# Kernel tuning notes

Hardware: AMD Instinct MI355X
Metric: run time of the kernel (lower is better)

The kernel has to match this reference:

```python
import jax, jax.numpy as jnp
import numpy as np

EPS = 1e-5
L = 8      # n_layers
H = 1024   # n_hidden
F_IN = 26  # input features
B = 65536  # batch


def layer_norm(x, gamma, beta):
    m = jnp.mean(x, axis=-1, keepdims=True)
    v = jnp.mean((x - m) ** 2, axis=-1, keepdims=True)
    return (x - m) * jax.lax.rsqrt(v + EPS) * gamma + beta


def setup_inputs() -> dict:
    key = jax.random.key(0)
    ks = jax.random.split(key, 12)
    s_in = 1.0 / np.sqrt(F_IN)
    s_h = 1.0 / np.sqrt(H)
    return {
        "x": jax.random.normal(ks[0], (B, F_IN), jnp.float32),
        "st_gamma": jnp.ones((F_IN,), jnp.float32),
        "st_beta": jnp.zeros((F_IN,), jnp.float32),
        "st_w": jax.random.uniform(ks[1], (H, F_IN), jnp.float32, -s_in, s_in),
        "st_b": jax.random.uniform(ks[2], (H,), jnp.float32, -s_in, s_in),
        "blk_gamma": jnp.ones((L, H), jnp.float32),
        "blk_beta": jnp.zeros((L, H), jnp.float32),
        "blk_w": jax.random.uniform(ks[3], (L, H, H), jnp.float32, -s_h, s_h),
        "blk_b": jax.random.uniform(ks[4], (L, H), jnp.float32, -s_h, s_h),
        "last_gamma": jnp.ones((H,), jnp.float32),
        "last_beta": jnp.zeros((H,), jnp.float32),
        "last_w": jax.random.uniform(ks[5], (1, H), jnp.float32, -s_h, s_h),
        "last_b": jax.random.uniform(ks[6], (1,), jnp.float32, -s_h, s_h),
    }


def reference(x, st_gamma, st_beta, st_w, st_b,
              blk_gamma, blk_beta, blk_w, blk_b,
              last_gamma, last_beta, last_w, last_b):
    # Stem: LN(26) -> Linear(26->H) -> ReLU (dropout = identity in eval)
    h = jax.nn.relu(layer_norm(x, st_gamma, st_beta) @ st_w.T + st_b)

    # n_layers blocks: LN -> Linear(H->H) -> ReLU, scanned over stacked params
    def body(h, params):
        g, b, w, bb = params
        h = jax.nn.relu(layer_norm(h, g, b) @ w.T + bb)
        return h, None

    h, _ = jax.lax.scan(body, h, (blk_gamma, blk_beta, blk_w, blk_b))

    # Head: LN -> Linear(H->1) -> sigmoid
    h = layer_norm(h, last_gamma, last_beta)
    out = jax.nn.sigmoid(h @ last_w.T + last_b)  # [B, 1]
    return out
```

## Files before the change

kernel.cpp:

```cpp
#include <hip/hip_runtime.h>
#include <hip/hip_bf16.h>
#include <stdint.h>


typedef __attribute__((ext_vector_type(8))) _Float16 f16x8;
typedef __attribute__((ext_vector_type(4))) float f32x4;

#define EPSLN 1e-5f
#define HDIM 1024

__device__ __forceinline__ void gload16(const void* g, void* l) {
  __builtin_amdgcn_global_load_lds(
      (const __attribute__((address_space(1))) unsigned int*)g,
      (__attribute__((address_space(3))) unsigned int*)l, 16, 0, 0);
}

__global__ __launch_bounds__(256) void zero_f32(float* __restrict__ p, int n) {
  int i = blockIdx.x * 256 + threadIdx.x;
  if (i < n) p[i] = 0.f;
}

__global__ __launch_bounds__(256) void fold_blk(
    const float* __restrict__ bg, const float* __restrict__ bb,
    const float* __restrict__ bw, const float* __restrict__ bbias,
    _Float16* __restrict__ Wf, float* __restrict__ bfold, float* __restrict__ Sfold) {
  int lo = blockIdx.x;
  int layer = lo >> 10;
  const float* wrow = bw + (size_t)lo * HDIM;
  const float* g = bg + (size_t)layer * HDIM;
  const float* be = bb + (size_t)layer * HDIM;
  _Float16* wout = Wf + (size_t)lo * HDIM;
  int t = threadIdx.x;
  float s = 0.f, acb = 0.f;
  for (int i = t; i < HDIM; i += 256) {
    float wv = wrow[i];
    _Float16 wp = (_Float16)(wv * g[i]);
    wout[i] = wp;
    s += (float)wp;
    acb += be[i] * wv;
  }
#pragma unroll
  for (int off = 1; off < 64; off <<= 1) { s += __shfl_xor(s, off); acb += __shfl_xor(acb, off); }
  __shared__ float rs[4], rb[4];
  int l = t & 63, w = t >> 6;
  if (l == 0) { rs[w] = s; rb[w] = acb; }
  __syncthreads();
  if (t == 0) {
    Sfold[lo] = rs[0] + rs[1] + rs[2] + rs[3];
    bfold[lo] = bbias[lo] + rb[0] + rb[1] + rb[2] + rb[3];
  }
}

__global__ __launch_bounds__(256) void fold_head(
    const float* __restrict__ lg, const float* __restrict__ lb,
    const float* __restrict__ lw, const float* __restrict__ lbias,
    float* __restrict__ headW, float* __restrict__ headAux) {
  int t = threadIdx.x;
  float s = 0.f, acb = 0.f;
  for (int i = t; i < HDIM; i += 256) {
    float wp = lw[i] * lg[i];
    headW[i] = wp;
    s += wp;
    acb += lb[i] * lw[i];
  }
#pragma unroll
  for (int off = 1; off < 64; off <<= 1) { s += __shfl_xor(s, off); acb += __shfl_xor(acb, off); }
  __shared__ float rs[4], rb[4];
  int l = t & 63, w = t >> 6;
  if (l == 0) { rs[w] = s; rb[w] = acb; }
  __syncthreads();
  if (t == 0) {
    headAux[0] = rs[0] + rs[1] + rs[2] + rs[3];
    headAux[1] = lbias[0] + rb[0] + rb[1] + rb[2] + rb[3];
  }
}

__global__ __launch_bounds__(256) void fold_stem(const float* __restrict__ stw,
                                                 _Float16* __restrict__ Wst) {
  int idx = blockIdx.x * 256 + threadIdx.x;
  int o = idx >> 6, i = idx & 63;
  Wst[idx] = (i < 26) ? (_Float16)stw[o * 26 + i] : (_Float16)0.f;
}

__global__ __launch_bounds__(256) void stem_prep(
    const float* __restrict__ x, const float* __restrict__ stg, const float* __restrict__ stb,
    _Float16* __restrict__ xn, int rowBase) {
  __shared__ float xin[256 * 26];
  __shared__ _Float16 xo[256 * 64];
  int t = threadIdx.x;
  const float* src = x + ((size_t)rowBase + (size_t)blockIdx.x * 256) * 26;
  for (int i = t; i < 256 * 26; i += 256) xin[i] = src[i];
  __syncthreads();
  {
    float m = 0.f;
#pragma unroll
    for (int i = 0; i < 26; ++i) m += xin[t * 26 + i];
    m *= (1.f / 26.f);
    float v = 0.f;
#pragma unroll
    for (int i = 0; i < 26; ++i) { float d = xin[t * 26 + i] - m; v += d * d; }
    float rstd = rsqrtf(v * (1.f / 26.f) + EPSLN);
    _Float16* orow = xo + t * 64;
#pragma unroll
    for (int i = 0; i < 26; ++i)
      orow[i] = (_Float16)((xin[t * 26 + i] - m) * rstd * stg[i] + stb[i]);
#pragma unroll
    for (int i = 26; i < 64; ++i) orow[i] = (_Float16)0.f;
  }
  __syncthreads();
  const float4* s4 = (const float4*)xo;
  float4* d4 = (float4*)(xn + (size_t)blockIdx.x * 256 * 64);
  for (int i = t; i < 2048; i += 256) d4[i] = s4[i];
}

__global__ __launch_bounds__(256) void stem_gemm(
    const _Float16* __restrict__ xn, const _Float16* __restrict__ Wst,
    const float* __restrict__ stbias, _Float16* __restrict__ hout,
    float* __restrict__ stats_out) {
  __shared__ _Float16 As[128 * 64];
  __shared__ _Float16 Bs[128 * 64];
  const int t = threadIdx.x;
  const int l = t & 63;
  const int w = t >> 6;
  const int wm = w >> 1, wn = w & 1;
  const int brow = blockIdx.x * 128;
  const int bcol = blockIdx.y * 128;

  f32x4 acc[4][4];
#pragma unroll
  for (int i = 0; i < 4; ++i)
#pragma unroll
    for (int j = 0; j < 4; ++j) acc[i][j] = (f32x4){0.f, 0.f, 0.f, 0.f};

  const _Float16* ga = xn + (size_t)(brow + (t >> 3)) * 64 + (t & 7) * 8;
  const _Float16* gb = Wst + (size_t)(bcol + (t >> 3)) * 64 + (t & 7) * 8;
  char* lA = (char*)As + (size_t)w * 1024;
  char* lB = (char*)Bs + (size_t)w * 1024;
#pragma unroll
  for (int q = 0; q < 4; ++q) {
    gload16(ga + (size_t)q * 32 * 64, lA + q * 4096);
    gload16(gb + (size_t)q * 32 * 64, lB + q * 4096);
  }
  __syncthreads();

  const int abyte0 = (wm * 64 + (l & 15)) * 128 + (l >> 4) * 16;
  const int bbyte0 = (wn * 64 + (l & 15)) * 128 + (l >> 4) * 16;
#pragma unroll
  for (int ks = 0; ks < 2; ++ks) {
    f16x8 af[4], bfr[4];
#pragma unroll
    for (int m = 0; m < 4; ++m)
      af[m] = *(const f16x8*)((const char*)As + abyte0 + m * 2048 + ks * 64);
#pragma unroll
    for (int n = 0; n < 4; ++n)
      bfr[n] = *(const f16x8*)((const char*)Bs + bbyte0 + n * 2048 + ks * 64);
#pragma unroll
    for (int m = 0; m < 4; ++m)
#pragma unroll
      for (int n = 0; n < 4; ++n)
        acc[m][n] = __builtin_amdgcn_mfma_f32_16x16x32_f16(af[m], bfr[n], acc[m][n], 0, 0, 0);
  }

  __syncthreads();
  float* sred = (float*)As;
  sred[t] = 0.f;
  __syncthreads();

  float Bf[4];
#pragma unroll
  for (int n = 0; n < 4; ++n) Bf[n] = stbias[bcol + wn * 64 + n * 16 + (l & 15)];
#pragma unroll
  for (int m = 0; m < 4; ++m) {
#pragma unroll
    for (int rg = 0; rg < 4; ++rg) {
      int rloc = wm * 64 + m * 16 + (l >> 4) * 4 + rg;
      int lrow = brow + rloc;
      float ps = 0.f, psq = 0.f;
#pragma unroll
      for (int n = 0; n < 4; ++n) {
        int col = bcol + wn * 64 + n * 16 + (l & 15);
        float vv = fmaxf(acc[m][n][rg] + Bf[n], 0.f);
        hout[(size_t)lrow * HDIM + col] = (_Float16)vv;
        ps += vv; psq += vv * vv;
      }
#pragma unroll
      for (int off = 1; off < 16; off <<= 1) {
        ps += __shfl_xor(ps, off);
        psq += __shfl_xor(psq, off);
      }
      if ((l & 15) == 0) {
        atomicAdd(&sred[rloc * 2 + 0], ps);
        atomicAdd(&sred[rloc * 2 + 1], psq);
      }
    }
  }
  __syncthreads();
  atomicAdd(&stats_out[(size_t)(brow + (t >> 1)) * 2 + (t & 1)], sred[t]);
}

__global__ __launch_bounds__(512, 2) void layer_gemm(
    const _Float16* __restrict__ hin, const float* __restrict__ stats_in,
    const _Float16* __restrict__ W, const float* __restrict__ bfold,
    const float* __restrict__ Sfold, _Float16* __restrict__ hout,
    float* __restrict__ stats_out) {
  __shared__ __align__(128) char smem[4 * 32768];
  const int t = threadIdx.x;
  const int l = t & 63;
  const int w = t >> 6;
  const int wm = w >> 2, wn = w & 3;
  int bid = blockIdx.x;
  {
    int nb = gridDim.x;
    if ((nb & 7) == 0) { int cpx = nb >> 3; bid = (bid & 7) * cpx + (bid >> 3); }
  }
  const int brow = (bid >> 2) * 256;
  const int bcol = (bid & 3) * 256;

  f32x4 acc[8][4];
#pragma unroll
  for (int i = 0; i < 8; ++i)
#pragma unroll
    for (int j = 0; j < 4; ++j) acc[i][j] = (f32x4){0.f, 0.f, 0.f, 0.f};

  const int cswz = (t & 3) ^ ((t >> 2) & 3);
  const _Float16* gA = hin + (size_t)(brow + (t >> 2)) * HDIM + cswz * 8;
  const _Float16* gB = W + (size_t)(bcol + (t >> 2)) * HDIM + cswz * 8;
  const int dstw = w << 10;

  auto stage = [&](int kt) {
    char* dA = smem + (kt & 3) * 32768 + dstw;
    const _Float16* sA = gA + kt * 32;
    const _Float16* sB = gB + kt * 32;
    gload16(sA, dA);
    gload16(sA + (size_t)128 * HDIM, dA + 8192);
    gload16(sB, dA + 16384);
    gload16(sB + (size_t)128 * HDIM, dA + 24576);
  };

  const int cxk = (((l >> 4) ^ (l & 3)) << 4);
  const int arow0 = wm * 8192 + (l & 15) * 64 + cxk;
  const int brow0 = 16384 + wn * 4096 + (l & 15) * 64 + cxk;

  auto tile = [&](int kt, bool do_stage) {
    const char* bc = smem + (kt & 3) * 32768;
    f16x8 bf[4], af[8];
#pragma unroll
    for (int n = 0; n < 4; ++n) bf[n] = *(const f16x8*)(bc + brow0 + n * 1024);
#pragma unroll
    for (int m = 0; m < 8; ++m) af[m] = *(const f16x8*)(bc + arow0 + m * 1024);
    if (do_stage) stage(kt + 3);
    __builtin_amdgcn_s_setprio(1);
#pragma unroll
    for (int m = 0; m < 8; ++m)
#pragma unroll
      for (int n = 0; n < 4; ++n)
        acc[m][n] = __builtin_amdgcn_mfma_f32_16x16x32_f16(af[m], bf[n], acc[m][n], 0, 0, 0);
    __builtin_amdgcn_s_setprio(0);
  };

#define TILE_BARRIER(N)                                      \
  do {                                                       \
    __builtin_amdgcn_sched_barrier(0);                       \
    asm volatile("s_waitcnt vmcnt(" #N ")" ::: "memory");    \
    __builtin_amdgcn_s_barrier();                            \
    __builtin_amdgcn_sched_barrier(0);                       \
  } while (0)

  stage(0);
  stage(1);
  stage(2);
  TILE_BARRIER(8);

#pragma unroll 1
  for (int kt = 0; kt < 29; ++kt) {
    tile(kt, true);
    TILE_BARRIER(8);
  }
  tile(29, false);
  TILE_BARRIER(4);
  tile(30, false);
  TILE_BARRIER(0);
  tile(31, false);
  __syncthreads();
#undef TILE_BARRIER

  float* sred = (float*)smem;
  sred[t] = 0.f;
  __syncthreads();

  float Sf[4], Bf2[4];
#pragma unroll
  for (int n = 0; n < 4; ++n) {
    int col = bcol + wn * 64 + n * 16 + (l & 15);
    Sf[n] = Sfold[col];
    Bf2[n] = bfold[col];
  }
#pragma unroll
  for (int m = 0; m < 8; ++m) {
#pragma unroll
    for (int rg = 0; rg < 4; ++rg) {
      int rloc = wm * 128 + m * 16 + (l >> 4) * 4 + rg;
      int grow = brow + rloc;
      float sum = stats_in[(size_t)grow * 2 + 0];
      float sumsq = stats_in[(size_t)grow * 2 + 1];
      float mean = sum * (1.f / 1024.f);
      float rstd = rsqrtf(sumsq * (1.f / 1024.f) - mean * mean + EPSLN);
      float ps = 0.f, psq = 0.f;
#pragma unroll
      for (int n = 0; n < 4; ++n) {
        int col = bcol + wn * 64 + n * 16 + (l & 15);
        float vv = rstd * (acc[m][n][rg] - mean * Sf[n]) + Bf2[n];
        vv = fmaxf(vv, 0.f);
        hout[(size_t)grow * HDIM + col] = (_Float16)vv;
        ps += vv; psq += vv * vv;
      }
#pragma unroll
      for (int off2 = 1; off2 < 16; off2 <<= 1) {
        ps += __shfl_xor(ps, off2);
        psq += __shfl_xor(psq, off2);
      }
      if ((l & 15) == 0) {
        atomicAdd(&sred[rloc * 2 + 0], ps);
        atomicAdd(&sred[rloc * 2 + 1], psq);
      }
    }
  }
  __syncthreads();
  atomicAdd(&stats_out[(size_t)(brow + (t >> 1)) * 2 + (t & 1)], sred[t]);
}

__global__ __launch_bounds__(512) void head_kernel(
    const _Float16* __restrict__ h8, const float* __restrict__ stats8,
    const float* __restrict__ headW, const float* __restrict__ headAux,
    float* __restrict__ out, int rowBase) {
  int t = threadIdx.x, l = t & 63, w = t >> 6;
  int lrow = blockIdx.x * 8 + w;
  const f16x8* hp = (const f16x8*)(h8 + (size_t)lrow * HDIM) + l * 2;
  f16x8 v0 = hp[0], v1 = hp[1];
  float acc = 0.f;
#pragma unroll
  for (int j = 0; j < 8; ++j) acc += (float)v0[j] * headW[l * 16 + j];
#pragma unroll
  for (int j = 0; j < 8; ++j) acc += (float)v1[j] * headW[l * 16 + 8 + j];
#pragma unroll
  for (int off = 1; off < 64; off <<= 1) acc += __shfl_xor(acc, off);
  if (l == 0) {
    float sum = stats8[lrow * 2 + 0], sumsq = stats8[lrow * 2 + 1];
    float mean = sum * (1.f / 1024.f);
    float rstd = rsqrtf(sumsq * (1.f / 1024.f) - mean * mean + EPSLN);
    float z = rstd * (acc - mean * headAux[0]) + headAux[1];
    out[rowBase + lrow] = 1.f / (1.f + expf(-z));
  }
}

extern "C" void kernel_launch(void* const* d_in, const int* in_sizes, int n_in,
                              void* d_out, int out_size, void* d_ws, size_t ws_size,
                              hipStream_t stream) {
  const float* x      = (const float*)d_in[0];
  const float* stg    = (const float*)d_in[1];
  const float* stb    = (const float*)d_in[2];
  const float* stw    = (const float*)d_in[3];
  const float* stbias = (const float*)d_in[4];
  const float* bg     = (const float*)d_in[5];
  const float* bb     = (const float*)d_in[6];
  const float* bw     = (const float*)d_in[7];
  const float* bbias  = (const float*)d_in[8];
  const float* lg     = (const float*)d_in[9];
  const float* lb     = (const float*)d_in[10];
  const float* lw     = (const float*)d_in[11];
  const float* lbias  = (const float*)d_in[12];
  float* out = (float*)d_out;
  const int B = 65536;
  const int L = 8;

  char* ws = (char*)d_ws;
  size_t off = 0;
  auto carve = [&](size_t bytes) -> char* {
    char* p = ws + off;
    off = (off + bytes + 255) & ~(size_t)255;
    return p;
  };
  _Float16* Wf   = (_Float16*)carve((size_t)L * HDIM * HDIM * 2);
  float* bfold   = (float*)carve((size_t)L * HDIM * 4);
  float* Sfold   = (float*)carve((size_t)L * HDIM * 4);
  float* headW   = (float*)carve((size_t)HDIM * 4);
  float* headAux = (float*)carve(256);
  _Float16* Wst  = (_Float16*)carve((size_t)HDIM * 64 * 2);
  size_t fixed = off;

  int R = B;
  while (R > 256) {
    size_t need = fixed + 2 * ((size_t)R * HDIM * 2 + 256) + ((size_t)9 * R * 2 * 4 + 256)
                  + ((size_t)R * 64 * 2 + 256);
    if (need <= ws_size) break;
    R >>= 1;
  }
  _Float16* hA = (_Float16*)carve((size_t)R * HDIM * 2);
  _Float16* hB = (_Float16*)carve((size_t)R * HDIM * 2);
  float* stats = (float*)carve((size_t)9 * R * 2 * 4);
  _Float16* xnb = (_Float16*)carve((size_t)R * 64 * 2);

  fold_blk<<<L * HDIM, 256, 0, stream>>>(bg, bb, bw, bbias, Wf, bfold, Sfold);
  fold_head<<<1, 256, 0, stream>>>(lg, lb, lw, lbias, headW, headAux);
  fold_stem<<<HDIM * 64 / 256, 256, 0, stream>>>(stw, Wst);

  const int nstats = 9 * R * 2;
  for (int c = 0; c < B / R; ++c) {
    int rowBase = c * R;
    zero_f32<<<(nstats + 255) / 256, 256, 0, stream>>>(stats, nstats);
    stem_prep<<<R / 256, 256, 0, stream>>>(x, stg, stb, xnb, rowBase);
    {
      dim3 grid(R / 128, 8);
      stem_gemm<<<grid, 256, 0, stream>>>(xnb, Wst, stbias, hA, stats);
    }
    _Float16* cur = hA;
    _Float16* nxt = hB;
    for (int lyr = 0; lyr < L; ++lyr) {
      int nb = (R / 256) * 4;
      layer_gemm<<<nb, 512, 0, stream>>>(
          cur, stats + (size_t)lyr * R * 2, Wf + (size_t)lyr * HDIM * HDIM,
          bfold + lyr * HDIM, Sfold + lyr * HDIM, nxt, stats + (size_t)(lyr + 1) * R * 2);
      _Float16* tmp = cur; cur = nxt; nxt = tmp;
    }
    head_kernel<<<R / 8, 512, 0, stream>>>(cur, stats + (size_t)8 * R * 2, headW, headAux, out, rowBase);
  }
}
```

Measured before the change: 1.419 ms.

## Fuse stem LayerNorm into stem GEMM and retune LDS swizzles

Removes the separate stem_prep kernel and its fp16 intermediate buffer: each stem_gemm block now loads its 128 input rows, computes the 26-feature LayerNorm in-block, and writes swizzled fp16 rows straight into LDS. The stem weight layout is pre-swizzled to match. The layer_gemm LDS XOR swizzle pattern is also changed to reduce bank conflicts. The cost is that the LayerNorm is recomputed by each of the 8 column blocks.

```diff
diff --git a/kernel.cpp b/kernel.cpp
--- a/kernel.cpp
+++ b/kernel.cpp
@@ -78,45 +78,16 @@
 __global__ __launch_bounds__(256) void fold_stem(const float* __restrict__ stw,
                                                  _Float16* __restrict__ Wst) {
   int idx = blockIdx.x * 256 + threadIdx.x;
-  int o = idx >> 6, i = idx & 63;
+  int o = idx >> 6, j = idx & 63;
+  int i = (((j >> 3) ^ (o & 7)) << 3) + (j & 7);
   Wst[idx] = (i < 26) ? (_Float16)stw[o * 26 + i] : (_Float16)0.f;
 }
 
-__global__ __launch_bounds__(256) void stem_prep(
+__global__ __launch_bounds__(256) void stem_gemm(
     const float* __restrict__ x, const float* __restrict__ stg, const float* __restrict__ stb,
-    _Float16* __restrict__ xn, int rowBase) {
-  __shared__ float xin[256 * 26];
-  __shared__ _Float16 xo[256 * 64];
-  int t = threadIdx.x;
-  const float* src = x + ((size_t)rowBase + (size_t)blockIdx.x * 256) * 26;
-  for (int i = t; i < 256 * 26; i += 256) xin[i] = src[i];
-  __syncthreads();
-  {
-    float m = 0.f;
-#pragma unroll
-    for (int i = 0; i < 26; ++i) m += xin[t * 26 + i];
-    m *= (1.f / 26.f);
-    float v = 0.f;
-#pragma unroll
-    for (int i = 0; i < 26; ++i) { float d = xin[t * 26 + i] - m; v += d * d; }
-    float rstd = rsqrtf(v * (1.f / 26.f) + EPSLN);
-    _Float16* orow = xo + t * 64;
-#pragma unroll
-    for (int i = 0; i < 26; ++i)
-      orow[i] = (_Float16)((xin[t * 26 + i] - m) * rstd * stg[i] + stb[i]);
-#pragma unroll
-    for (int i = 26; i < 64; ++i) orow[i] = (_Float16)0.f;
-  }
-  __syncthreads();
-  const float4* s4 = (const float4*)xo;
-  float4* d4 = (float4*)(xn + (size_t)blockIdx.x * 256 * 64);
-  for (int i = t; i < 2048; i += 256) d4[i] = s4[i];
-}
-
-__global__ __launch_bounds__(256) void stem_gemm(
-    const _Float16* __restrict__ xn, const _Float16* __restrict__ Wst,
-    const float* __restrict__ stbias, _Float16* __restrict__ hout,
-    float* __restrict__ stats_out) {
+    const _Float16* __restrict__ Wst, const float* __restrict__ stbias,
+    _Float16* __restrict__ hout, float* __restrict__ stats_out, int rowBase) {
+  __shared__ float xin[128 * 26];
   __shared__ _Float16 As[128 * 64];
   __shared__ _Float16 Bs[128 * 64];
   const int t = threadIdx.x;
@@ -126,34 +97,60 @@
   const int brow = blockIdx.x * 128;
   const int bcol = blockIdx.y * 128;
 
+  const _Float16* gb = Wst + (size_t)(bcol + (t >> 3)) * 64 + (t & 7) * 8;
+  char* lB = (char*)Bs + (size_t)w * 1024;
+#pragma unroll
+  for (int q = 0; q < 4; ++q) gload16(gb + (size_t)q * 32 * 64, lB + q * 4096);
+
+  const float* src = x + ((size_t)rowBase + brow) * 26;
+  for (int i = t; i < 128 * 26; i += 256) xin[i] = src[i];
+  __syncthreads();
+
+  if (t < 128) {
+    float m = 0.f;
+#pragma unroll
+    for (int i = 0; i < 26; ++i) m += xin[t * 26 + i];
+    m *= (1.f / 26.f);
+    float v = 0.f;
+#pragma unroll
+    for (int i = 0; i < 26; ++i) { float d = xin[t * 26 + i] - m; v += d * d; }
+    float rstd = rsqrtf(v * (1.f / 26.f) + EPSLN);
+    _Float16 tmp[32];
+#pragma unroll
+    for (int i = 0; i < 26; ++i)
+      tmp[i] = (_Float16)((xin[t * 26 + i] - m) * rstd * stg[i] + stb[i]);
+#pragma unroll
+    for (int i = 26; i < 32; ++i) tmp[i] = (_Float16)0.f;
+    char* arow = (char*)As + t * 128;
+#pragma unroll
+    for (int c = 0; c < 4; ++c) {
+      f16x8 vv;
+#pragma unroll
+      for (int j = 0; j < 8; ++j) vv[j] = tmp[c * 8 + j];
+      *(f16x8*)(arow + ((c ^ (t & 7)) << 4)) = vv;
+    }
+    f16x8 vz = (f16x8)(_Float16)0.f;
+#pragma unroll
+    for (int c = 4; c < 8; ++c) *(f16x8*)(arow + ((c ^ (t & 7)) << 4)) = vz;
+  }
+  __syncthreads();
+
   f32x4 acc[4][4];
 #pragma unroll
   for (int i = 0; i < 4; ++i)
 #pragma unroll
     for (int j = 0; j < 4; ++j) acc[i][j] = (f32x4){0.f, 0.f, 0.f, 0.f};
 
-  const _Float16* ga = xn + (size_t)(brow + (t >> 3)) * 64 + (t & 7) * 8;
-  const _Float16* gb = Wst + (size_t)(bcol + (t >> 3)) * 64 + (t & 7) * 8;
-  char* lA = (char*)As + (size_t)w * 1024;
-  char* lB = (char*)Bs + (size_t)w * 1024;
-#pragma unroll
-  for (int q = 0; q < 4; ++q) {
-    gload16(ga + (size_t)q * 32 * 64, lA + q * 4096);
-    gload16(gb + (size_t)q * 32 * 64, lB + q * 4096);
-  }
-  __syncthreads();
-
-  const int abyte0 = (wm * 64 + (l & 15)) * 128 + (l >> 4) * 16;
-  const int bbyte0 = (wn * 64 + (l & 15)) * 128 + (l >> 4) * 16;
 #pragma unroll
   for (int ks = 0; ks < 2; ++ks) {
+    const int cx = ((ks * 4 + (l >> 4)) ^ (l & 7)) << 4;
     f16x8 af[4], bfr[4];
 #pragma unroll
     for (int m = 0; m < 4; ++m)
-      af[m] = *(const f16x8*)((const char*)As + abyte0 + m * 2048 + ks * 64);
+      af[m] = *(const f16x8*)((const char*)As + (wm * 64 + m * 16 + (l & 15)) * 128 + cx);
 #pragma unroll
     for (int n = 0; n < 4; ++n)
-      bfr[n] = *(const f16x8*)((const char*)Bs + bbyte0 + n * 2048 + ks * 64);
+      bfr[n] = *(const f16x8*)((const char*)Bs + (wn * 64 + n * 16 + (l & 15)) * 128 + cx);
 #pragma unroll
     for (int m = 0; m < 4; ++m)
 #pragma unroll
@@ -162,8 +159,8 @@
   }
 
   __syncthreads();
-  float* sred = (float*)As;
-  sred[t] = 0.f;
+  float* sred = (float*)xin;
+  if (t < 256) sred[t] = 0.f;
   __syncthreads();
 
   float Bf[4];
@@ -195,7 +192,7 @@
     }
   }
   __syncthreads();
-  atomicAdd(&stats_out[(size_t)(brow + (t >> 1)) * 2 + (t & 1)], sred[t]);
+  if (t < 256) atomicAdd(&stats_out[(size_t)(brow + (t >> 1)) * 2 + (t & 1)], sred[t]);
 }
 
 __global__ __launch_bounds__(512, 2) void layer_gemm(
@@ -222,7 +219,7 @@
 #pragma unroll
     for (int j = 0; j < 4; ++j) acc[i][j] = (f32x4){0.f, 0.f, 0.f, 0.f};
 
-  const int cswz = (t & 3) ^ ((t >> 2) & 3);
+  const int cswz = (t & 3) ^ ((t >> 3) & 3);
   const _Float16* gA = hin + (size_t)(brow + (t >> 2)) * HDIM + cswz * 8;
   const _Float16* gB = W + (size_t)(bcol + (t >> 2)) * HDIM + cswz * 8;
   const int dstw = w << 10;
@@ -237,7 +234,7 @@
     gload16(sB + (size_t)128 * HDIM, dA + 24576);
   };
 
-  const int cxk = (((l >> 4) ^ (l & 3)) << 4);
+  const int cxk = (((l >> 4) ^ (((l & 15) >> 1) & 3)) << 4);
   const int arow0 = wm * 8192 + (l & 15) * 64 + cxk;
   const int brow0 = 16384 + wn * 4096 + (l & 15) * 64 + cxk;
 
@@ -390,15 +387,13 @@
 
   int R = B;
   while (R > 256) {
-    size_t need = fixed + 2 * ((size_t)R * HDIM * 2 + 256) + ((size_t)9 * R * 2 * 4 + 256)
-                  + ((size_t)R * 64 * 2 + 256);
+    size_t need = fixed + 2 * ((size_t)R * HDIM * 2 + 256) + ((size_t)9 * R * 2 * 4 + 256);
     if (need <= ws_size) break;
     R >>= 1;
   }
   _Float16* hA = (_Float16*)carve((size_t)R * HDIM * 2);
   _Float16* hB = (_Float16*)carve((size_t)R * HDIM * 2);
   float* stats = (float*)carve((size_t)9 * R * 2 * 4);
-  _Float16* xnb = (_Float16*)carve((size_t)R * 64 * 2);
 
   fold_blk<<<L * HDIM, 256, 0, stream>>>(bg, bb, bw, bbias, Wf, bfold, Sfold);
   fold_head<<<1, 256, 0, stream>>>(lg, lb, lw, lbias, headW, headAux);
@@ -408,10 +403,9 @@
   for (int c = 0; c < B / R; ++c) {
     int rowBase = c * R;
     zero_f32<<<(nstats + 255) / 256, 256, 0, stream>>>(stats, nstats);
-    stem_prep<<<R / 256, 256, 0, stream>>>(x, stg, stb, xnb, rowBase);
     {
       dim3 grid(R / 128, 8);
-      stem_gemm<<<grid, 256, 0, stream>>>(xnb, Wst, stbias, hA, stats);
+      stem_gemm<<<grid, 256, 0, stream>>>(x, stg, stb, Wst, stbias, hA, stats, rowBase);
     }
     _Float16* cur = hA;
     _Float16* nxt = hB;
```

New measurement: 1.396 ms. No clear change (-1.6%).
